# Optimization experiments

Hardware: AMD Instinct MI355X
Metric: run time of the kernel (lower is better)

The kernel has to match this reference:

```python
import jax, jax.numpy as jnp
import numpy as np
import math

B, S, D, H = 4, 2048, 1024, 16
HD = D // H
EPS = 1e-10


def setup_inputs() -> dict:
    key = jax.random.key(0)
    kx, kq, kk, kv, ko = jax.random.split(key, 5)
    x = jax.random.normal(kx, (B, S, D), dtype=jnp.float32)
    # causal additive mask: 0 on/below diagonal, -1e9 above
    mask = jnp.where(jnp.triu(jnp.ones((S, S), dtype=bool), k=1), -1e9, 0.0).astype(jnp.float32)
    scale = 1.0 / math.sqrt(D)
    Wq = jax.random.normal(kq, (D, D), dtype=jnp.float32) * scale
    Wk = jax.random.normal(kk, (D, D), dtype=jnp.float32) * scale
    Wv = jax.random.normal(kv, (D, D), dtype=jnp.float32) * scale
    Wo = jax.random.normal(ko, (D, D), dtype=jnp.float32) * scale
    return {"x": x, "mask": mask, "Wq": Wq, "Wk": Wk, "Wv": Wv, "Wo": Wo}


def _nirmalya_softmax(t):
    # faithful to original: plain exp (no max-subtraction), eps in denominator
    p1 = jnp.exp(t)
    return p1 / (jnp.sum(p1, axis=-1, keepdims=True) + EPS)


def reference(x, mask, Wq, Wk, Wv, Wo):
    b, s, d = x.shape
    # torch Linear (bias=False): y = x @ W.T
    def proj(W):
        y = jnp.einsum('bsd,ed->bse', x, W)
        return y.reshape(b, s, H, HD).transpose(0, 2, 1, 3)  # [b,h,s,hd]
    q, k, v = proj(Wq), proj(Wk), proj(Wv)
    scores = jnp.einsum('bhqd,bhkd->bhqk', q, k) / math.sqrt(HD)
    scores = scores + mask  # broadcast over batch/heads
    attn = _nirmalya_softmax(scores)
    out = jnp.einsum('bhqk,bhkd->bhqd', attn, v)
    out = out.transpose(0, 2, 1, 3).reshape(b, s, d)
    return jnp.einsum('bsd,ed->bse', out, Wo)
```

## Files before the change

kernel.cpp:

```cpp
#include <hip/hip_runtime.h>
#include <hip/hip_bf16.h>

typedef __bf16 bf16;
typedef __attribute__((ext_vector_type(8))) __bf16 bf16x8;
typedef __attribute__((ext_vector_type(4))) float f32x4;
typedef __attribute__((ext_vector_type(16))) float f32x16;
typedef __attribute__((ext_vector_type(2))) unsigned int u32x2;
typedef __attribute__((ext_vector_type(4))) unsigned int u32x4;

#define MFMA16(a, b, c) __builtin_amdgcn_mfma_f32_16x16x32_bf16((a), (b), (c), 0, 0, 0)
#define MFMA32(a, b, c) __builtin_amdgcn_mfma_f32_32x32x16_bf16((a), (b), (c), 0, 0, 0)

#define GLOAD_LDS16(gp, lp)                                                              \
  __builtin_amdgcn_global_load_lds(                                                      \
      (const __attribute__((address_space(1))) unsigned int*)(gp),                       \
      (__attribute__((address_space(3))) unsigned int*)(lp), 16, 0, 0)

#define BAR()   __builtin_amdgcn_s_barrier()
#define LGKM0() asm volatile("s_waitcnt lgkmcnt(0)" ::: "memory")
#define VMC(n)  asm volatile("s_waitcnt vmcnt(" #n ")" ::: "memory")
#define PRIO1() __builtin_amdgcn_s_setprio(1)
#define PRIO0() __builtin_amdgcn_s_setprio(0)

__global__ __launch_bounds__(256) void cvt_all(const float* __restrict__ x,
                                               const float* __restrict__ wq,
                                               const float* __restrict__ wk,
                                               const float* __restrict__ wv,
                                               const float* __restrict__ wo,
                                               bf16* __restrict__ xb,
                                               bf16* __restrict__ wqkv,
                                               bf16* __restrict__ wob) {
  constexpr int NXC = 8388608 / 8;
  constexpr int NWC = 1048576 / 8;
  constexpr int TOT = NXC + 4 * NWC;
  for (int c = blockIdx.x * 256 + threadIdx.x; c < TOT; c += gridDim.x * 256) {
    const float* src; bf16* dst; int idx;
    if (c < NXC) { src = x; dst = xb; idx = c; }
    else {
      int c2 = c - NXC; int wsel = c2 >> 17; idx = c2 & (NWC - 1);
      src = wsel == 0 ? wq : wsel == 1 ? wk : wsel == 2 ? wv : wo;
      dst = wsel < 3 ? wqkv + (size_t)wsel * 1048576 : wob;
    }
    float4 v0 = reinterpret_cast<const float4*>(src)[idx * 2];
    float4 v1 = reinterpret_cast<const float4*>(src)[idx * 2 + 1];
    bf16x8 o;
    o[0] = (bf16)v0.x; o[1] = (bf16)v0.y; o[2] = (bf16)v0.z; o[3] = (bf16)v0.w;
    o[4] = (bf16)v1.x; o[5] = (bf16)v1.y; o[6] = (bf16)v1.z; o[7] = (bf16)v1.w;
    reinterpret_cast<bf16x8*>(dst)[idx] = o;
  }
}

#define MMAC(MH)                                                                         \
  _Pragma("unroll") for (int mi = 0; mi < 2; ++mi)                                       \
  _Pragma("unroll") for (int ni = 0; ni < 2; ++ni)                                       \
  _Pragma("unroll") for (int ks = 0; ks < 2; ++ks)                                       \
      acc[(MH) * 2 + mi][ni] =                                                           \
          MFMA16(af[(MH) * 2 + mi][ks], bfr[ni][ks], acc[(MH) * 2 + mi][ni]);

template <int MODE, int NT>
__global__ __launch_bounds__(512, 4) void gemm8c(const bf16* __restrict__ A,
                                                 const bf16* __restrict__ B,
                                                 void* __restrict__ Cv,
                                                 bf16* __restrict__ VT) {
  constexpr int K = 1024;
  __shared__ bf16 smem[32768];
  bf16* Asm = smem;
  bf16* Bsm = smem + 16384;
  const int tid = threadIdx.x, lane = tid & 63, w = tid >> 6;
  const int l15 = lane & 15, l16 = lane >> 4;
  const int wr = w >> 2, wc = w & 3;
  const int lin = blockIdx.x;
  const int idx = lin >> 3;
  const int mt = (lin & 7) * 8 + idx / NT;
  const int nt = idx % NT;
  const int bm0 = mt * 128, bn0 = nt * 128;

  auto stage = [&](int t, int buf) {
#pragma unroll
    for (int j = 0; j < 2; ++j) {
      const int r = j * 64 + (tid >> 3);
      const int g = (tid & 7) ^ (r & 7);
      GLOAD_LDS16(&A[(size_t)(bm0 + r) * K + t * 64 + g * 8],
                  &Asm[buf * 8192 + j * 4096 + tid * 8]);
    }
#pragma unroll
    for (int j = 0; j < 2; ++j) {
      const int r = j * 64 + (tid >> 3);
      const int g = (tid & 7) ^ (r & 7);
      GLOAD_LDS16(&B[(size_t)(bn0 + r) * K + t * 64 + g * 8],
                  &Bsm[buf * 8192 + j * 4096 + tid * 8]);
    }
  };

  bf16x8 af[4][2], bfr[2][2];
  auto ldAll = [&](int buf) {
#pragma unroll
    for (int f = 0; f < 4; ++f)
#pragma unroll
      for (int ks = 0; ks < 2; ++ks)
        af[f][ks] = *reinterpret_cast<const bf16x8*>(
            &Asm[buf * 8192 + (wr * 64 + f * 16 + l15) * 64 +
                 (((ks * 4 + l16) ^ (l15 & 7)) * 8)]);
#pragma unroll
    for (int ni = 0; ni < 2; ++ni)
#pragma unroll
      for (int ks = 0; ks < 2; ++ks)
        bfr[ni][ks] = *reinterpret_cast<const bf16x8*>(
            &Bsm[buf * 8192 + (wc * 32 + ni * 16 + l15) * 64 +
                 (((ks * 4 + l16) ^ (l15 & 7)) * 8)]);
  };

  f32x4 acc[4][2] = {};

  stage(0, 0); stage(1, 1);
  VMC(4); BAR();

#pragma unroll 1
  for (int it = 0; it < K / 128; ++it) {
    const int t0 = 2 * it;
    const bool last = (it == K / 128 - 1);
    ldAll(0);
    BAR(); LGKM0();
    PRIO1(); MMAC(0); PRIO0();
    BAR();
    if (!last) stage(t0 + 2, 0);
    PRIO1(); MMAC(1); PRIO0();
    if (last) { VMC(0); } else { VMC(4); }
    BAR();
    ldAll(1);
    BAR(); LGKM0();
    PRIO1(); MMAC(0); PRIO0();
    BAR();
    if (!last) stage(t0 + 3, 1);
    PRIO1(); MMAC(1); PRIO0();
    if (!last) VMC(4);
    BAR();
  }

  if constexpr (MODE == 0) {
#pragma unroll
    for (int f = 0; f < 4; ++f)
#pragma unroll
      for (int ni = 0; ni < 2; ++ni)
#pragma unroll
        for (int rr = 0; rr < 4; ++rr) {
          const size_t row = bm0 + wr * 64 + f * 16 + l16 * 4 + rr;
          const size_t col = bn0 + wc * 32 + ni * 16 + l15;
          reinterpret_cast<float*>(Cv)[row * (NT * 128) + col] = acc[f][ni][rr];
        }
  } else {
    if (bn0 < 2048) {
#pragma unroll
      for (int f = 0; f < 4; ++f)
#pragma unroll
        for (int ni = 0; ni < 2; ++ni)
#pragma unroll
          for (int rr = 0; rr < 4; ++rr) {
            const size_t row = bm0 + wr * 64 + f * 16 + l16 * 4 + rr;
            const size_t col = bn0 + wc * 32 + ni * 16 + l15;
            float v = acc[f][ni][rr];
            if (col < 1024) v *= 0.18033688011112042f;
            reinterpret_cast<bf16*>(Cv)[row * 2048 + col] = (bf16)v;
          }
    } else {
      BAR();
#pragma unroll
      for (int f = 0; f < 4; ++f)
#pragma unroll
        for (int ni = 0; ni < 2; ++ni)
#pragma unroll
          for (int rr = 0; rr < 4; ++rr) {
            const int ml = wr * 64 + f * 16 + l16 * 4 + rr;
            const int nl = wc * 32 + ni * 16 + l15;
            smem[nl * 136 + ml] = (bf16)acc[f][ni][rr];
          }
      BAR();
      const int n = tid >> 2, mseg = tid & 3;
      const size_t vb = ((size_t)(bm0 >> 11) * 1024 + (bn0 - 2048 + n)) * 2048 +
                        (bm0 & 2047) + mseg * 32;
#pragma unroll
      for (int k = 0; k < 4; ++k) {
        bf16x8 v = *reinterpret_cast<const bf16x8*>(&smem[n * 136 + mseg * 32 + k * 8]);
        *reinterpret_cast<bf16x8*>(&VT[vb + k * 8]) = v;
      }
    }
  }
}

constexpr int S_ = 2048, H_ = 16, LDQK = 2048;

__global__ __launch_bounds__(256, 2) void attn_kernel(const bf16* __restrict__ QK,
                                                      const bf16* __restrict__ VT,
                                                      bf16* __restrict__ AO) {
  __shared__ bf16 Ks[2][64 * 64];
  __shared__ bf16 Vs[2][64 * 64];
  const int tid = threadIdx.x, lane = tid & 63, w = tid >> 6;
  const int l31 = lane & 31, hi = lane >> 5;
  const int x7 = l31 & 7;
  const int bh = blockIdx.x, b = bh >> 4, h = bh & (H_ - 1);
  const int pairid = blockIdx.y;
  const size_t qoff = (size_t)b * S_ * LDQK + h * 64;
  const size_t koff = qoff + 1024;
  const size_t voff = (size_t)bh * 64 * LDQK;
  const size_t aoff = (size_t)b * S_ * 1024 + h * 64;

  auto stK = [&](int t) {
    const int kv0 = t * 64, bs = t & 1;
#pragma unroll
    for (int i = 0; i < 2; ++i) {
      const int c = tid + 256 * i;
      const int row = c >> 3, gs = (c & 7) ^ (row & 7);
      GLOAD_LDS16(&QK[koff + (size_t)(kv0 + row) * LDQK + gs * 8], &Ks[bs][c * 8]);
    }
  };
  auto stV = [&](int t) {
    const int kv0 = t * 64, bs = t & 1;
#pragma unroll
    for (int i = 0; i < 2; ++i) {
      const int c = tid + 256 * i;
      const int row = c >> 3, gs = (c & 7) ^ (row & 7);
      GLOAD_LDS16(&VT[voff + (size_t)row * LDQK + kv0 + gs * 8], &Vs[bs][c * 8]);
    }
  };

#pragma unroll 1
  for (int half = 0; half < 2; ++half) {
    const int j = half ? (15 - pairid) : pairid;
    const int qbase = j * 128 + w * 32;
    const int ntiles = 2 * j + 2;
    const int tmax = (qbase + 31) >> 6;
    const int qg = qbase + l31;

    bf16x8 qf[4];
#pragma unroll
    for (int ks = 0; ks < 4; ++ks)
      qf[ks] = *reinterpret_cast<const bf16x8*>(
          &QK[qoff + (size_t)qg * LDQK + ks * 16 + hi * 8]);

    f32x16 oT[2] = {};
    float rsq[4] = {0.f, 0.f, 0.f, 0.f};
    f32x16 scA[2], scB[2];

    auto qkt = [&](int t, f32x16 (&sc)[2]) {
      const int bs = t & 1;
      f32x16 zz = {};
      sc[0] = zz; sc[1] = zz;
      PRIO1();
#pragma unroll
      for (int ks = 0; ks < 4; ++ks) {
        bf16x8 kf0 = *reinterpret_cast<bf16x8*>(
            &Ks[bs][l31 * 64 + (((ks * 2 + hi) ^ x7) * 8)]);
        bf16x8 kf1 = *reinterpret_cast<bf16x8*>(
            &Ks[bs][(32 + l31) * 64 + (((ks * 2 + hi) ^ x7) * 8)]);
        sc[0] = MFMA32(kf0, qf[ks], sc[0]);
        sc[1] = MFMA32(kf1, qf[ks], sc[1]);
      }
      PRIO0();
    };

    auto softpv = [&](int t, f32x16 (&sc)[2]) {
      const bool msk = (t >= tmax);
      const int kv0 = t * 64;
      const int hi4 = hi * 4;
#pragma unroll
      for (int hh = 0; hh < 2; ++hh)
#pragma unroll
        for (int r = 0; r < 16; ++r) {
          float e;
          asm("v_exp_f32 %0, %1" : "=v"(e) : "v"(sc[hh][r]));
          if (msk) {
            const int kvg = kv0 + hh * 32 + (r & 3) + 8 * (r >> 2) + hi4;
            e = (kvg <= qg) ? e : 0.0f;
          }
          rsq[r & 3] += e;
          sc[hh][r] = e;
        }
      u32x4 pf[4];
#pragma unroll
      for (int hh = 0; hh < 2; ++hh)
#pragma unroll
        for (int q4 = 0; q4 < 2; ++q4) {
          unsigned x0, x1, y0, y1;
          asm("v_cvt_pk_bf16_f32 %0, %1, %2" : "=v"(x0)
              : "v"(sc[hh][q4 * 8 + 0]), "v"(sc[hh][q4 * 8 + 1]));
          asm("v_cvt_pk_bf16_f32 %0, %1, %2" : "=v"(x1)
              : "v"(sc[hh][q4 * 8 + 2]), "v"(sc[hh][q4 * 8 + 3]));
          asm("v_cvt_pk_bf16_f32 %0, %1, %2" : "=v"(y0)
              : "v"(sc[hh][q4 * 8 + 4]), "v"(sc[hh][q4 * 8 + 5]));
          asm("v_cvt_pk_bf16_f32 %0, %1, %2" : "=v"(y1)
              : "v"(sc[hh][q4 * 8 + 6]), "v"(sc[hh][q4 * 8 + 7]));
          asm("v_permlane32_swap_b32 %0, %1" : "+v"(x0), "+v"(y0));
          asm("v_permlane32_swap_b32 %0, %1" : "+v"(x1), "+v"(y1));
          pf[hh * 2 + q4][0] = x0; pf[hh * 2 + q4][1] = x1;
          pf[hh * 2 + q4][2] = y0; pf[hh * 2 + q4][3] = y1;
        }
      const int bs = t & 1;
      PRIO1();
#pragma unroll
      for (int ks = 0; ks < 4; ++ks) {
        bf16x8 vt0 = *reinterpret_cast<bf16x8*>(
            &Vs[bs][l31 * 64 + (((ks * 2 + hi) ^ x7) * 8)]);
        bf16x8 vt1 = *reinterpret_cast<bf16x8*>(
            &Vs[bs][(32 + l31) * 64 + (((ks * 2 + hi) ^ x7) * 8)]);
        oT[0] = MFMA32(vt0, *reinterpret_cast<bf16x8*>(&pf[ks]), oT[0]);
        oT[1] = MFMA32(vt1, *reinterpret_cast<bf16x8*>(&pf[ks]), oT[1]);
      }
      PRIO0();
    };

    auto step = [&](int t, f32x16 (&cur)[2], f32x16 (&nxt)[2]) {
      if (t + 2 < ntiles) stK(t + 2);
      if (t + 1 < ntiles) { stV(t + 1); qkt(t + 1, nxt); }
      softpv(t, cur);
      VMC(0); BAR();
    };

    stK(0); stV(0);
    if (ntiles > 1) stK(1);
    VMC(0); BAR();
    qkt(0, scA);
    BAR();

#pragma unroll 1
    for (int t = 0; t < ntiles; t += 2) {
      step(t, scA, scB);
      if (t + 1 < ntiles) step(t + 1, scB, scA);
    }

    const float rsum = (rsq[0] + rsq[1]) + (rsq[2] + rsq[3]);
    const float rst = rsum + __shfl_xor(rsum, 32);
    const float inv = 1.0f / (rst + 1e-10f);

    bf16* lo = &Ks[0][0] + w * 2048;
#pragma unroll
    for (int dh = 0; dh < 2; ++dh)
#pragma unroll
      for (int rq = 0; rq < 4; ++rq) {
        const float v0 = oT[dh][rq * 4 + 0] * inv, v1 = oT[dh][rq * 4 + 1] * inv;
        const float v2 = oT[dh][rq * 4 + 2] * inv, v3 = oT[dh][rq * 4 + 3] * inv;
        unsigned d0, d1;
        asm("v_cvt_pk_bf16_f32 %0, %1, %2" : "=v"(d0) : "v"(v0), "v"(v1));
        asm("v_cvt_pk_bf16_f32 %0, %1, %2" : "=v"(d1) : "v"(v2), "v"(v3));
        u32x2 dd; dd[0] = d0; dd[1] = d1;
        *reinterpret_cast<u32x2*>(
            &lo[l31 * 64 + (((dh * 4 + rq) ^ x7) * 8) + hi * 4]) = dd;
      }
#pragma unroll
    for (int jj = 0; jj < 4; ++jj) {
      const int gran = lane + 64 * jj;
      const int qr = gran >> 3, g = gran & 7;
      bf16x8 vv = *reinterpret_cast<bf16x8*>(&lo[qr * 64 + ((g ^ (qr & 7)) * 8)]);
      *reinterpret_cast<bf16x8*>(
          &AO[aoff + (size_t)(qbase - w * 32 + w * 32 + qr) * 1024 + g * 8]) = vv;
    }
    LGKM0(); BAR();
  }
}

extern "C" void kernel_launch(void* const* d_in, const int* in_sizes, int n_in,
                              void* d_out, int out_size, void* d_ws, size_t ws_size,
                              hipStream_t stream) {
  const float* x  = (const float*)d_in[0];
  const float* Wq = (const float*)d_in[2];
  const float* Wk = (const float*)d_in[3];
  const float* Wv = (const float*)d_in[4];
  const float* Wo = (const float*)d_in[5];

  constexpr int B = 4, S = 2048, D = 1024;
  constexpr size_t nx = (size_t)B * S * D;
  constexpr size_t nw = (size_t)D * D;

  char* ws = (char*)d_ws;
  bf16* xb    = (bf16*)ws;
  bf16* Wqkvb = xb + nx;
  bf16* Wob   = Wqkvb + 3 * nw;
  bf16* QKb   = Wob + nw;
  bf16* VTb   = QKb + (size_t)B * S * 2048;
  bf16* AOb   = VTb + nx;

  cvt_all<<<2048, 256, 0, stream>>>(x, Wq, Wk, Wv, Wo, xb, Wqkvb, Wob);

  gemm8c<2, 24><<<1536, 512, 0, stream>>>(xb, Wqkvb, QKb, VTb);

  attn_kernel<<<dim3(B * H_, 8), 256, 0, stream>>>(QKb, VTb, AOb);

  gemm8c<0, 8><<<512, 512, 0, stream>>>(AOb, Wob, d_out, nullptr);
}
```

Baseline: 152.7 us.

## Tile K/V into contiguous 64x64 blocks and use single-wave attention blocks reading global directly

The QKV GEMM epilogue now writes Q to its own buffer and stores K and V^T as contiguous 64x64 tiles per (batch, head, kv-tile). The attention kernel becomes a one-wavefront block per 32 query rows that loads K and V fragments straight from global memory (relying on cache), with no LDS staging, barriers or software pipelining. This aims to remove barrier and LDS-staging overhead and to raise parallelism from 512 to 4096 blocks, with the heaviest query blocks scheduled first. The cost is redundant global/L2 reads of K and V across waves and no explicit latency hiding for those loads. The K epilogue also becomes scattered 2-byte stores.

```diff
diff --git a/kernel.cpp b/kernel.cpp
--- a/kernel.cpp
+++ b/kernel.cpp
@@ -61,7 +61,8 @@
 __global__ __launch_bounds__(512, 4) void gemm8c(const bf16* __restrict__ A,
                                                  const bf16* __restrict__ B,
                                                  void* __restrict__ Cv,
-                                                 bf16* __restrict__ VT) {
+                                                 bf16* __restrict__ KT,
+                                                 bf16* __restrict__ V2) {
   constexpr int K = 1024;
   __shared__ bf16 smem[32768];
   bf16* Asm = smem;
@@ -149,7 +150,7 @@
           reinterpret_cast<float*>(Cv)[row * (NT * 128) + col] = acc[f][ni][rr];
         }
   } else {
-    if (bn0 < 2048) {
+    if (bn0 < 1024) {
 #pragma unroll
       for (int f = 0; f < 4; ++f)
 #pragma unroll
@@ -158,9 +159,21 @@
           for (int rr = 0; rr < 4; ++rr) {
             const size_t row = bm0 + wr * 64 + f * 16 + l16 * 4 + rr;
             const size_t col = bn0 + wc * 32 + ni * 16 + l15;
-            float v = acc[f][ni][rr];
-            if (col < 1024) v *= 0.18033688011112042f;
-            reinterpret_cast<bf16*>(Cv)[row * 2048 + col] = (bf16)v;
+            reinterpret_cast<bf16*>(Cv)[row * 1024 + col] =
+                (bf16)(acc[f][ni][rr] * 0.18033688011112042f);
+          }
+    } else if (bn0 < 2048) {
+#pragma unroll
+      for (int f = 0; f < 4; ++f)
+#pragma unroll
+        for (int ni = 0; ni < 2; ++ni)
+#pragma unroll
+          for (int rr = 0; rr < 4; ++rr) {
+            const int row = bm0 + wr * 64 + f * 16 + l16 * 4 + rr;
+            const int col = bn0 + wc * 32 + ni * 16 + l15;
+            const int bh2 = ((row >> 11) << 4) + ((col - 1024) >> 6);
+            KT[((size_t)bh2 * 32 + ((row & 2047) >> 6)) * 4096 +
+               (row & 63) * 64 + (col & 63)] = (bf16)acc[f][ni][rr];
           }
     } else {
       BAR();
@@ -176,184 +189,137 @@
           }
       BAR();
       const int n = tid >> 2, mseg = tid & 3;
-      const size_t vb = ((size_t)(bm0 >> 11) * 1024 + (bn0 - 2048 + n)) * 2048 +
-                        (bm0 & 2047) + mseg * 32;
+      const int dg = bn0 - 2048 + n;
+      const int bh2 = ((bm0 >> 11) << 4) + (dg >> 6);
+      const int tt = ((bm0 & 2047) >> 6) + (mseg >> 1);
+      const size_t vb = ((size_t)bh2 * 32 + tt) * 4096 + (dg & 63) * 64 +
+                        (mseg & 1) * 32;
 #pragma unroll
       for (int k = 0; k < 4; ++k) {
         bf16x8 v = *reinterpret_cast<const bf16x8*>(&smem[n * 136 + mseg * 32 + k * 8]);
-        *reinterpret_cast<bf16x8*>(&VT[vb + k * 8]) = v;
+        *reinterpret_cast<bf16x8*>(&V2[vb + k * 8]) = v;
       }
     }
   }
 }
 
-constexpr int S_ = 2048, H_ = 16, LDQK = 2048;
-
-__global__ __launch_bounds__(256, 2) void attn_kernel(const bf16* __restrict__ QK,
-                                                      const bf16* __restrict__ VT,
-                                                      bf16* __restrict__ AO) {
-  __shared__ bf16 Ks[2][64 * 64];
-  __shared__ bf16 Vs[2][64 * 64];
-  const int tid = threadIdx.x, lane = tid & 63, w = tid >> 6;
+constexpr int S_ = 2048, H_ = 16;
+
+__global__ __launch_bounds__(64, 3) void attn_kernel(const bf16* __restrict__ Qb,
+                                                     const bf16* __restrict__ KT,
+                                                     const bf16* __restrict__ V2,
+                                                     bf16* __restrict__ AO) {
+  __shared__ bf16 lo[32 * 64];
+  const int lane = threadIdx.x;
   const int l31 = lane & 31, hi = lane >> 5;
   const int x7 = l31 & 7;
   const int bh = blockIdx.x, b = bh >> 4, h = bh & (H_ - 1);
-  const int pairid = blockIdx.y;
-  const size_t qoff = (size_t)b * S_ * LDQK + h * 64;
-  const size_t koff = qoff + 1024;
-  const size_t voff = (size_t)bh * 64 * LDQK;
-  const size_t aoff = (size_t)b * S_ * 1024 + h * 64;
-
-  auto stK = [&](int t) {
-    const int kv0 = t * 64, bs = t & 1;
-#pragma unroll
-    for (int i = 0; i < 2; ++i) {
-      const int c = tid + 256 * i;
-      const int row = c >> 3, gs = (c & 7) ^ (row & 7);
-      GLOAD_LDS16(&QK[koff + (size_t)(kv0 + row) * LDQK + gs * 8], &Ks[bs][c * 8]);
-    }
-  };
-  auto stV = [&](int t) {
-    const int kv0 = t * 64, bs = t & 1;
-#pragma unroll
-    for (int i = 0; i < 2; ++i) {
-      const int c = tid + 256 * i;
-      const int row = c >> 3, gs = (c & 7) ^ (row & 7);
-      GLOAD_LDS16(&VT[voff + (size_t)row * LDQK + kv0 + gs * 8], &Vs[bs][c * 8]);
-    }
-  };
+  const int s = 63 - blockIdx.y;
+  const int qbase = s * 32;
+  const int ntiles = ((qbase + 31) >> 6) + 1;
+  const int qg = qbase + l31;
+  const size_t qoff = (size_t)b * S_ * 1024 + h * 64;
+  const bf16* ktb = KT + (size_t)bh * 32 * 4096;
+  const bf16* vtb = V2 + (size_t)bh * 32 * 4096;
+
+  bf16x8 qf[4];
+#pragma unroll
+  for (int ks = 0; ks < 4; ++ks)
+    qf[ks] = *reinterpret_cast<const bf16x8*>(
+        &Qb[qoff + (size_t)qg * 1024 + ks * 16 + hi * 8]);
+
+  f32x16 oT[2] = {};
+  float rsq[4] = {0.f, 0.f, 0.f, 0.f};
 
 #pragma unroll 1
-  for (int half = 0; half < 2; ++half) {
-    const int j = half ? (15 - pairid) : pairid;
-    const int qbase = j * 128 + w * 32;
-    const int ntiles = 2 * j + 2;
-    const int tmax = (qbase + 31) >> 6;
-    const int qg = qbase + l31;
-
-    bf16x8 qf[4];
-#pragma unroll
-    for (int ks = 0; ks < 4; ++ks)
-      qf[ks] = *reinterpret_cast<const bf16x8*>(
-          &QK[qoff + (size_t)qg * LDQK + ks * 16 + hi * 8]);
-
-    f32x16 oT[2] = {};
-    float rsq[4] = {0.f, 0.f, 0.f, 0.f};
-    f32x16 scA[2], scB[2];
-
-    auto qkt = [&](int t, f32x16 (&sc)[2]) {
-      const int bs = t & 1;
-      f32x16 zz = {};
-      sc[0] = zz; sc[1] = zz;
-      PRIO1();
-#pragma unroll
-      for (int ks = 0; ks < 4; ++ks) {
-        bf16x8 kf0 = *reinterpret_cast<bf16x8*>(
-            &Ks[bs][l31 * 64 + (((ks * 2 + hi) ^ x7) * 8)]);
-        bf16x8 kf1 = *reinterpret_cast<bf16x8*>(
-            &Ks[bs][(32 + l31) * 64 + (((ks * 2 + hi) ^ x7) * 8)]);
-        sc[0] = MFMA32(kf0, qf[ks], sc[0]);
-        sc[1] = MFMA32(kf1, qf[ks], sc[1]);
+  for (int t = 0; t < ntiles; ++t) {
+    const bf16* kt = ktb + t * 4096;
+    f32x16 sc[2] = {};
+    PRIO1();
+#pragma unroll
+    for (int ks = 0; ks < 4; ++ks) {
+      bf16x8 kf0 = *reinterpret_cast<const bf16x8*>(
+          &kt[l31 * 64 + (ks * 2 + hi) * 8]);
+      bf16x8 kf1 = *reinterpret_cast<const bf16x8*>(
+          &kt[(32 + l31) * 64 + (ks * 2 + hi) * 8]);
+      sc[0] = MFMA32(kf0, qf[ks], sc[0]);
+      sc[1] = MFMA32(kf1, qf[ks], sc[1]);
+    }
+    PRIO0();
+
+    const bool msk = (t == ntiles - 1);
+    const int kv0 = t * 64;
+    const int hi4 = hi * 4;
+#pragma unroll
+    for (int hh = 0; hh < 2; ++hh)
+#pragma unroll
+      for (int r = 0; r < 16; ++r) {
+        float e;
+        asm("v_exp_f32 %0, %1" : "=v"(e) : "v"(sc[hh][r]));
+        if (msk) {
+          const int kvg = kv0 + hh * 32 + (r & 3) + 8 * (r >> 2) + hi4;
+          e = (kvg <= qg) ? e : 0.0f;
+        }
+        rsq[r & 3] += e;
+        sc[hh][r] = e;
       }
-      PRIO0();
-    };
-
-    auto softpv = [&](int t, f32x16 (&sc)[2]) {
-      const bool msk = (t >= tmax);
-      const int kv0 = t * 64;
-      const int hi4 = hi * 4;
-#pragma unroll
-      for (int hh = 0; hh < 2; ++hh)
-#pragma unroll
-        for (int r = 0; r < 16; ++r) {
-          float e;
-          asm("v_exp_f32 %0, %1" : "=v"(e) : "v"(sc[hh][r]));
-          if (msk) {
-            const int kvg = kv0 + hh * 32 + (r & 3) + 8 * (r >> 2) + hi4;
-            e = (kvg <= qg) ? e : 0.0f;
-          }
-          rsq[r & 3] += e;
-          sc[hh][r] = e;
-        }
-      u32x4 pf[4];
-#pragma unroll
-      for (int hh = 0; hh < 2; ++hh)
-#pragma unroll
-        for (int q4 = 0; q4 < 2; ++q4) {
-          unsigned x0, x1, y0, y1;
-          asm("v_cvt_pk_bf16_f32 %0, %1, %2" : "=v"(x0)
-              : "v"(sc[hh][q4 * 8 + 0]), "v"(sc[hh][q4 * 8 + 1]));
-          asm("v_cvt_pk_bf16_f32 %0, %1, %2" : "=v"(x1)
-              : "v"(sc[hh][q4 * 8 + 2]), "v"(sc[hh][q4 * 8 + 3]));
-          asm("v_cvt_pk_bf16_f32 %0, %1, %2" : "=v"(y0)
-              : "v"(sc[hh][q4 * 8 + 4]), "v"(sc[hh][q4 * 8 + 5]));
-          asm("v_cvt_pk_bf16_f32 %0, %1, %2" : "=v"(y1)
-              : "v"(sc[hh][q4 * 8 + 6]), "v"(sc[hh][q4 * 8 + 7]));
-          asm("v_permlane32_swap_b32 %0, %1" : "+v"(x0), "+v"(y0));
-          asm("v_permlane32_swap_b32 %0, %1" : "+v"(x1), "+v"(y1));
-          pf[hh * 2 + q4][0] = x0; pf[hh * 2 + q4][1] = x1;
-          pf[hh * 2 + q4][2] = y0; pf[hh * 2 + q4][3] = y1;
-        }
-      const int bs = t & 1;
-      PRIO1();
-#pragma unroll
-      for (int ks = 0; ks < 4; ++ks) {
-        bf16x8 vt0 = *reinterpret_cast<bf16x8*>(
-            &Vs[bs][l31 * 64 + (((ks * 2 + hi) ^ x7) * 8)]);
-        bf16x8 vt1 = *reinterpret_cast<bf16x8*>(
-            &Vs[bs][(32 + l31) * 64 + (((ks * 2 + hi) ^ x7) * 8)]);
-        oT[0] = MFMA32(vt0, *reinterpret_cast<bf16x8*>(&pf[ks]), oT[0]);
-        oT[1] = MFMA32(vt1, *reinterpret_cast<bf16x8*>(&pf[ks]), oT[1]);
+    u32x4 pf[4];
+#pragma unroll
+    for (int hh = 0; hh < 2; ++hh)
+#pragma unroll
+      for (int q4 = 0; q4 < 2; ++q4) {
+        unsigned x0, x1, y0, y1;
+        asm("v_cvt_pk_bf16_f32 %0, %1, %2" : "=v"(x0)
+            : "v"(sc[hh][q4 * 8 + 0]), "v"(sc[hh][q4 * 8 + 1]));
+        asm("v_cvt_pk_bf16_f32 %0, %1, %2" : "=v"(x1)
+            : "v"(sc[hh][q4 * 8 + 2]), "v"(sc[hh][q4 * 8 + 3]));
+        asm("v_cvt_pk_bf16_f32 %0, %1, %2" : "=v"(y0)
+            : "v"(sc[hh][q4 * 8 + 4]), "v"(sc[hh][q4 * 8 + 5]));
+        asm("v_cvt_pk_bf16_f32 %0, %1, %2" : "=v"(y1)
+            : "v"(sc[hh][q4 * 8 + 6]), "v"(sc[hh][q4 * 8 + 7]));
+        asm("v_permlane32_swap_b32 %0, %1" : "+v"(x0), "+v"(y0));
+        asm("v_permlane32_swap_b32 %0, %1" : "+v"(x1), "+v"(y1));
+        pf[hh * 2 + q4][0] = x0; pf[hh * 2 + q4][1] = x1;
+        pf[hh * 2 + q4][2] = y0; pf[hh * 2 + q4][3] = y1;
       }
-      PRIO0();
-    };
-
-    auto step = [&](int t, f32x16 (&cur)[2], f32x16 (&nxt)[2]) {
-      if (t + 2 < ntiles) stK(t + 2);
-      if (t + 1 < ntiles) { stV(t + 1); qkt(t + 1, nxt); }
-      softpv(t, cur);
-      VMC(0); BAR();
-    };
-
-    stK(0); stV(0);
-    if (ntiles > 1) stK(1);
-    VMC(0); BAR();
-    qkt(0, scA);
-    BAR();
-
-#pragma unroll 1
-    for (int t = 0; t < ntiles; t += 2) {
-      step(t, scA, scB);
-      if (t + 1 < ntiles) step(t + 1, scB, scA);
-    }
-
-    const float rsum = (rsq[0] + rsq[1]) + (rsq[2] + rsq[3]);
-    const float rst = rsum + __shfl_xor(rsum, 32);
-    const float inv = 1.0f / (rst + 1e-10f);
-
-    bf16* lo = &Ks[0][0] + w * 2048;
-#pragma unroll
-    for (int dh = 0; dh < 2; ++dh)
-#pragma unroll
-      for (int rq = 0; rq < 4; ++rq) {
-        const float v0 = oT[dh][rq * 4 + 0] * inv, v1 = oT[dh][rq * 4 + 1] * inv;
-        const float v2 = oT[dh][rq * 4 + 2] * inv, v3 = oT[dh][rq * 4 + 3] * inv;
-        unsigned d0, d1;
-        asm("v_cvt_pk_bf16_f32 %0, %1, %2" : "=v"(d0) : "v"(v0), "v"(v1));
-        asm("v_cvt_pk_bf16_f32 %0, %1, %2" : "=v"(d1) : "v"(v2), "v"(v3));
-        u32x2 dd; dd[0] = d0; dd[1] = d1;
-        *reinterpret_cast<u32x2*>(
-            &lo[l31 * 64 + (((dh * 4 + rq) ^ x7) * 8) + hi * 4]) = dd;
-      }
-#pragma unroll
-    for (int jj = 0; jj < 4; ++jj) {
-      const int gran = lane + 64 * jj;
-      const int qr = gran >> 3, g = gran & 7;
-      bf16x8 vv = *reinterpret_cast<bf16x8*>(&lo[qr * 64 + ((g ^ (qr & 7)) * 8)]);
-      *reinterpret_cast<bf16x8*>(
-          &AO[aoff + (size_t)(qbase - w * 32 + w * 32 + qr) * 1024 + g * 8]) = vv;
-    }
-    LGKM0(); BAR();
+    const bf16* vt = vtb + t * 4096;
+    PRIO1();
+#pragma unroll
+    for (int ks = 0; ks < 4; ++ks) {
+      bf16x8 vt0 = *reinterpret_cast<const bf16x8*>(
+          &vt[l31 * 64 + (ks * 2 + hi) * 8]);
+      bf16x8 vt1 = *reinterpret_cast<const bf16x8*>(
+          &vt[(32 + l31) * 64 + (ks * 2 + hi) * 8]);
+      oT[0] = MFMA32(vt0, *reinterpret_cast<bf16x8*>(&pf[ks]), oT[0]);
+      oT[1] = MFMA32(vt1, *reinterpret_cast<bf16x8*>(&pf[ks]), oT[1]);
+    }
+    PRIO0();
+  }
+
+  const float rsum = (rsq[0] + rsq[1]) + (rsq[2] + rsq[3]);
+  const float rst = rsum + __shfl_xor(rsum, 32);
+  const float inv = 1.0f / (rst + 1e-10f);
+
+#pragma unroll
+  for (int dh = 0; dh < 2; ++dh)
+#pragma unroll
+    for (int rq = 0; rq < 4; ++rq) {
+      const float v0 = oT[dh][rq * 4 + 0] * inv, v1 = oT[dh][rq * 4 + 1] * inv;
+      const float v2 = oT[dh][rq * 4 + 2] * inv, v3 = oT[dh][rq * 4 + 3] * inv;
+      unsigned d0, d1;
+      asm("v_cvt_pk_bf16_f32 %0, %1, %2" : "=v"(d0) : "v"(v0), "v"(v1));
+      asm("v_cvt_pk_bf16_f32 %0, %1, %2" : "=v"(d1) : "v"(v2), "v"(v3));
+      u32x2 dd; dd[0] = d0; dd[1] = d1;
+      *reinterpret_cast<u32x2*>(
+          &lo[l31 * 64 + (((dh * 4 + rq) ^ x7) * 8) + hi * 4]) = dd;
+    }
+#pragma unroll
+  for (int jj = 0; jj < 4; ++jj) {
+    const int gran = lane + 64 * jj;
+    const int qr = gran >> 3, g = gran & 7;
+    bf16x8 vv = *reinterpret_cast<bf16x8*>(&lo[qr * 64 + ((g ^ (qr & 7)) * 8)]);
+    *reinterpret_cast<bf16x8*>(
+        &AO[qoff + (size_t)(qbase + qr) * 1024 + g * 8]) = vv;
   }
 }
 
@@ -374,15 +340,16 @@
   bf16* xb    = (bf16*)ws;
   bf16* Wqkvb = xb + nx;
   bf16* Wob   = Wqkvb + 3 * nw;
-  bf16* QKb   = Wob + nw;
-  bf16* VTb   = QKb + (size_t)B * S * 2048;
-  bf16* AOb   = VTb + nx;
+  bf16* Qbuf  = Wob + nw;
+  bf16* KTb   = Qbuf + nx;
+  bf16* V2b   = KTb + nx;
+  bf16* AOb   = V2b + nx;
 
   cvt_all<<<2048, 256, 0, stream>>>(x, Wq, Wk, Wv, Wo, xb, Wqkvb, Wob);
 
-  gemm8c<2, 24><<<1536, 512, 0, stream>>>(xb, Wqkvb, QKb, VTb);
-
-  attn_kernel<<<dim3(B * H_, 8), 256, 0, stream>>>(QKb, VTb, AOb);
-
-  gemm8c<0, 8><<<512, 512, 0, stream>>>(AOb, Wob, d_out, nullptr);
+  gemm8c<2, 24><<<1536, 512, 0, stream>>>(xb, Wqkvb, Qbuf, KTb, V2b);
+
+  attn_kernel<<<dim3(B * H_, 64), 64, 0, stream>>>(Qbuf, KTb, V2b, AOb);
+
+  gemm8c<0, 8><<<512, 512, 0, stream>>>(AOb, Wob, d_out, nullptr, nullptr);
 }
```

Result: slower. 217.1 us (+42.2%).
